# Kernel optimization log

Hardware: AMD Instinct MI355X
Metric: run time of the kernel (lower is better)

The kernel has to match this reference:

```python
import jax, jax.numpy as jnp
import numpy as np

D_MODEL = 768
NUM_HEADS = 12
HEAD_DIM = D_MODEL // NUM_HEADS
SEQ = 4096
BATCH = 1


def setup_inputs() -> dict:
    key = jax.random.key(0)
    ks = jax.random.split(key, 6)
    scale = 1.0 / np.sqrt(D_MODEL)
    x = jax.random.normal(ks[0], (BATCH, SEQ, D_MODEL), dtype=jnp.float32)
    mask = jnp.tril(jnp.ones((SEQ, SEQ), dtype=bool))[None, None]  # [1,1,S,S] causal
    Wq = jax.random.normal(ks[1], (D_MODEL, D_MODEL), dtype=jnp.float32) * scale
    Wk = jax.random.normal(ks[2], (D_MODEL, D_MODEL), dtype=jnp.float32) * scale
    Wv = jax.random.normal(ks[3], (D_MODEL, D_MODEL), dtype=jnp.float32) * scale
    Wo = jax.random.normal(ks[4], (D_MODEL, D_MODEL), dtype=jnp.float32) * scale
    bo = jax.random.normal(ks[5], (D_MODEL,), dtype=jnp.float32) * 0.01
    return {"x": x, "mask": mask, "Wq": Wq, "Wk": Wk, "Wv": Wv, "Wo": Wo, "bo": bo}


def _rope_tables(seq_len, head_dim, dtype):
    # inv_freq over even dims; emb = cat(freqs, freqs) but only the first half
    # participates in the well-defined rotation (x1/x2 have head_dim//2 channels)
    inv_freq = 1.0 / (10000.0 ** (jnp.arange(0, head_dim, 2, dtype=dtype) / head_dim))
    t = jnp.arange(seq_len, dtype=dtype)
    freqs = t[:, None] * inv_freq[None, :]  # [S, head_dim//2]
    return jnp.cos(freqs), jnp.sin(freqs)


def _apply_rotary(xh, cos, sin):
    # xh: [B,H,S,hd]; cos/sin: [S, hd//2]
    x1 = xh[..., ::2]
    x2 = xh[..., 1::2]
    # faithful to source: concatenated (not interleaved) rotated halves
    return jnp.concatenate([x1 * cos - x2 * sin, x1 * sin + x2 * cos], axis=-1)


def reference(x, mask, Wq, Wk, Wv, Wo, bo):
    B, S, D = x.shape
    H, hd = NUM_HEADS, HEAD_DIM
    def split_heads(y):
        return y.reshape(B, S, H, hd).transpose(0, 2, 1, 3)  # [B,H,S,hd]
    q = split_heads(x @ Wq.T)
    k = split_heads(x @ Wk.T)
    v = split_heads(x @ Wv.T)
    cos, sin = _rope_tables(S, hd, x.dtype)
    q = _apply_rotary(q, cos, sin)
    k = _apply_rotary(k, cos, sin)
    scores = jnp.einsum('bhqd,bhkd->bhqk', q, k) / jnp.sqrt(jnp.asarray(hd, x.dtype))
    scores = jnp.where(mask, scores, jnp.asarray(-1e9, x.dtype))
    attn = jax.nn.softmax(scores, axis=-1)  # dropout is identity in eval
    out = jnp.einsum('bhqk,bhkd->bhqd', attn, v)
    out = out.transpose(0, 2, 1, 3).reshape(B, S, D)
    return out @ Wo.T + bo
```

## Files before the change

### kernel.cpp

```cpp
#include <hip/hip_runtime.h>
#include <hip/hip_bf16.h>
#include <math.h>

#define SEQ 4096
#define DM  768
#define NH  12
#define HD  64
#define PER ((size_t)NH * SEQ * HD)
#define XN  ((size_t)SEQ * DM)
#define WN  ((size_t)DM * DM)

typedef __attribute__((ext_vector_type(8))) short bf16x8;
typedef __attribute__((ext_vector_type(4))) short s16x4;
typedef __attribute__((ext_vector_type(4))) float f32x4;

#define MFMA(a, b, c) __builtin_amdgcn_mfma_f32_16x16x32_bf16((a), (b), (c), 0, 0, 0)

#if __has_builtin(__builtin_amdgcn_exp2f)
#define EXP2(x) __builtin_amdgcn_exp2f(x)
#else
#define EXP2(x) exp2f(x)
#endif

#define SWZ(row, blk) (((row) << 6) + ((((blk) ^ ((row) & 7))) << 3))

__device__ __forceinline__ unsigned short f2b(float f) {
    unsigned int u = __float_as_uint(f);
    u += 0x7FFFu + ((u >> 16) & 1u);
    return (unsigned short)(u >> 16);
}

__global__ __launch_bounds__(256) void prep_kernel(
    const float* __restrict__ x,  const float* __restrict__ wq,
    const float* __restrict__ wk, const float* __restrict__ wv,
    const float* __restrict__ wo,
    unsigned short* __restrict__ dstbase, float2* __restrict__ rope)
{
    const float* srcs[5] = {x, wq, wk, wv, wo};
    const size_t n4s[5]  = {XN / 4, WN / 4, WN / 4, WN / 4, WN / 4};
    unsigned short* d = dstbase;
    for (int rg = 0; rg < 5; ++rg) {
        const float4* s4 = (const float4*)srcs[rg];
        s16x4* d4 = (s16x4*)d;
        for (size_t i = (size_t)blockIdx.x * 256 + threadIdx.x; i < n4s[rg];
             i += (size_t)gridDim.x * 256) {
            const float4 v = s4[i];
            s16x4 p;
            p.x = (short)f2b(v.x); p.y = (short)f2b(v.y);
            p.z = (short)f2b(v.z); p.w = (short)f2b(v.w);
            d4[i] = p;
        }
        d += n4s[rg] * 4;
    }
    for (int g = blockIdx.x * 256 + threadIdx.x; g < 131072; g += gridDim.x * 256) {
        const int row = g >> 5, fi = g & 31;
        const float invf = expf(-(float)fi * 0.28782313662425576f);
        float sn, cs;
        sincosf((float)row * invf, &sn, &cs);
        rope[row * 32 + fi] = make_float2(cs, sn);
    }
}

__global__ __launch_bounds__(256) void qkv128(
    const float* __restrict__ x,  const unsigned short* __restrict__ xb,
    const float* __restrict__ Wq, const float* __restrict__ Wk, const float* __restrict__ Wv,
    const unsigned short* __restrict__ Wqb, const unsigned short* __restrict__ Wkb,
    const unsigned short* __restrict__ Wvb,
    const float2* __restrict__ rope,
    unsigned short* __restrict__ Qo, unsigned short* __restrict__ Ko,
    unsigned short* __restrict__ Vo, int fast)
{
    __shared__ __align__(16) unsigned short SMEM[32768];
    unsigned short* At0 = SMEM;
    unsigned short* At1 = SMEM + 8192;
    unsigned short* Bt0 = SMEM + 16384;
    unsigned short* Bt1 = SMEM + 24576;

    const int t    = threadIdx.x;
    const int w    = t >> 6;
    const int lane = t & 63;
    const int quad = lane >> 4;
    const int l16  = lane & 15;
    const int region = blockIdx.y / 6;
    const int ntile  = blockIdx.y % 6;
    const int n0 = ntile * 128;
    const int s0 = blockIdx.x * 128;
    const int m0  = 64 * (w & 1);
    const int nn0 = 64 * (w >> 1);

    const unsigned short* Wb = (region == 0) ? Wqb : (region == 1) ? Wkb : Wvb;
    const float*          Wf = (region == 0) ? Wq  : (region == 1) ? Wk  : Wv;

    f32x4 acc[4][4];
    #pragma unroll
    for (int i = 0; i < 4; ++i)
        #pragma unroll
        for (int j = 0; j < 4; ++j) acc[i][j] = (f32x4){0, 0, 0, 0};

    bf16x8 areg[4], breg[4];
    if (fast) {
        #pragma unroll
        for (int i = 0; i < 4; ++i) {
            const int s = t + i * 256, row = s >> 3, bp = s & 7, blk = bp ^ (row & 7);
            areg[i] = *(const bf16x8*)&xb[(size_t)(s0 + row) * DM + blk * 8];
            breg[i] = *(const bf16x8*)&Wb[(size_t)(n0 + row) * DM + blk * 8];
        }
        #pragma unroll
        for (int i = 0; i < 4; ++i) {
            const int s = t + i * 256, row = s >> 3, bp = s & 7;
            *(bf16x8*)&At0[row * 64 + bp * 8] = areg[i];
            *(bf16x8*)&Bt0[row * 64 + bp * 8] = breg[i];
        }
    } else {
        for (int e = t; e < 2048; e += 256) {
            const int row = e >> 4, c4 = e & 15;
            const int off = (row << 6) + (((c4 >> 1) ^ (row & 7)) << 3) + (c4 & 1) * 4;
            const float4 xv = *(const float4*)&x[(size_t)(s0 + row) * DM + c4 * 4];
            s16x4 px; px.x = (short)f2b(xv.x); px.y = (short)f2b(xv.y);
            px.z = (short)f2b(xv.z); px.w = (short)f2b(xv.w);
            *(s16x4*)&At0[off] = px;
            const float4 wv = *(const float4*)&Wf[(size_t)(n0 + row) * DM + c4 * 4];
            s16x4 pw; pw.x = (short)f2b(wv.x); pw.y = (short)f2b(wv.y);
            pw.z = (short)f2b(wv.z); pw.w = (short)f2b(wv.w);
            *(s16x4*)&Bt0[off] = pw;
        }
    }
    __syncthreads();

    for (int kt = 0; kt < 12; ++kt) {
        if (fast && kt < 11) {
            const int k0n = (kt + 1) * 64;
            #pragma unroll
            for (int i = 0; i < 4; ++i) {
                const int s = t + i * 256, row = s >> 3, bp = s & 7, blk = bp ^ (row & 7);
                areg[i] = *(const bf16x8*)&xb[(size_t)(s0 + row) * DM + k0n + blk * 8];
                breg[i] = *(const bf16x8*)&Wb[(size_t)(n0 + row) * DM + k0n + blk * 8];
            }
        }
        const unsigned short* Ab = (kt & 1) ? At1 : At0;
        const unsigned short* Bb = (kt & 1) ? Bt1 : Bt0;

        bf16x8 aA[4][2], bB[4][2];
        #pragma unroll
        for (int i = 0; i < 4; ++i)
            #pragma unroll
            for (int hh = 0; hh < 2; ++hh) {
                aA[i][hh] = *(const bf16x8*)&Ab[SWZ(m0 + 16 * i + l16, 4 * hh + quad)];
                bB[i][hh] = *(const bf16x8*)&Bb[SWZ(nn0 + 16 * i + l16, 4 * hh + quad)];
            }
        #pragma unroll
        for (int hh = 0; hh < 2; ++hh)
            #pragma unroll
            for (int i = 0; i < 4; ++i)
                #pragma unroll
                for (int j = 0; j < 4; ++j)
                    acc[i][j] = MFMA(aA[i][hh], bB[j][hh], acc[i][j]);

        if (kt < 11) {
            unsigned short* An = ((kt + 1) & 1) ? At1 : At0;
            unsigned short* Bn = ((kt + 1) & 1) ? Bt1 : Bt0;
            if (fast) {
                #pragma unroll
                for (int i = 0; i < 4; ++i) {
                    const int s = t + i * 256, row = s >> 3, bp = s & 7;
                    *(bf16x8*)&An[row * 64 + bp * 8] = areg[i];
                    *(bf16x8*)&Bn[row * 64 + bp * 8] = breg[i];
                }
            } else {
                const int k0n = (kt + 1) * 64;
                for (int e = t; e < 2048; e += 256) {
                    const int row = e >> 4, c4 = e & 15;
                    const int off = (row << 6) + (((c4 >> 1) ^ (row & 7)) << 3) + (c4 & 1) * 4;
                    const float4 xv = *(const float4*)&x[(size_t)(s0 + row) * DM + k0n + c4 * 4];
                    s16x4 px; px.x = (short)f2b(xv.x); px.y = (short)f2b(xv.y);
                    px.z = (short)f2b(xv.z); px.w = (short)f2b(xv.w);
                    *(s16x4*)&An[off] = px;
                    const float4 wv = *(const float4*)&Wf[(size_t)(n0 + row) * DM + k0n + c4 * 4];
                    s16x4 pw; pw.x = (short)f2b(wv.x); pw.y = (short)f2b(wv.y);
                    pw.z = (short)f2b(wv.z); pw.w = (short)f2b(wv.w);
                    *(s16x4*)&Bn[off] = pw;
                }
            }
        }
        __syncthreads();
    }

    if (region <= 1) {
        unsigned short* dst = (region == 0) ? Qo : Ko;
        const float qsc = (region == 0) ? 0.18033688011112042f : 1.0f;
        #pragma unroll
        for (int i = 0; i < 4; ++i)
            #pragma unroll
            for (int j = 0; j < 4; ++j)
                #pragma unroll
                for (int r = 0; r < 4; ++r) {
                    const int srow = s0 + m0 + 16 * i + 4 * quad + r;
                    const int n = n0 + nn0 + 16 * j + l16;
                    const int h = n >> 6, d = n & 63, fi = d >> 1;
                    const float own = acc[i][j][r] * qsc;
                    const float oth = __shfl_xor(own, 1);
                    float cs, sn;
                    if (fast) {
                        const float2 t2 = rope[srow * 32 + fi];
                        cs = t2.x; sn = t2.y;
                    } else {
                        const float invf = expf(-(float)fi * 0.28782313662425576f);
                        sincosf((float)srow * invf, &sn, &cs);
                    }
                    const float val = (d & 1) ? (oth * sn + own * cs)
                                              : (own * cs - oth * sn);
                    dst[(size_t)h * SEQ * HD + (size_t)srow * HD +
                        ((d & 1) ? 32 : 0) + fi] = f2b(val);
                }
    } else {
        unsigned short* VL = SMEM;
        #pragma unroll
        for (int i = 0; i < 4; ++i)
            #pragma unroll
            for (int j = 0; j < 4; ++j)
                #pragma unroll
                for (int r = 0; r < 4; ++r)
                    VL[(nn0 + 16 * j + l16) * 130 + m0 + 16 * i + 4 * quad + r] =
                        f2b(acc[i][j][r]);
        __syncthreads();
        for (int e = t; e < 8192; e += 256) {
            const int dl = e >> 6, sp = e & 63;
            const unsigned int v = (unsigned int)VL[dl * 130 + 2 * sp] |
                                   ((unsigned int)VL[dl * 130 + 2 * sp + 1] << 16);
            const int n = n0 + dl, h = n >> 6, d = n & 63;
            *(unsigned int*)&Vo[(size_t)h * SEQ * HD + (size_t)d * SEQ + s0 + 2 * sp] = v;
        }
    }
}

__global__ __launch_bounds__(256, 2) void attn_mfma(
    const unsigned short* __restrict__ Q,
    const unsigned short* __restrict__ K,
    const unsigned short* __restrict__ V,
    unsigned short* __restrict__ O,
    float* __restrict__ Part)
{
    __shared__ __align__(16) unsigned char SM[53248];
    unsigned short* Kst = (unsigned short*)SM;
    unsigned short* Vt  = (unsigned short*)(SM + 16384);
    unsigned short* Ps  = (unsigned short*)(SM + 32768);
    float* ACC  = (float*)SM;
    float* ACC2 = (float*)(SM + 32768);
    float* Lx   = (float*)(SM + 51200);

    const int h  = blockIdx.y;
    const int xx = blockIdx.x;
    int i, kstart, nch, domask, partial, pslice;
    if (gridDim.x == 96) {
        if (xx < 64) {
            i = 63 - xx; kstart = 0;
            const int full = ((i * 64 + 63) >> 7) + 1;
            nch = full < 16 ? full : 16;
            domask  = (i <= 31);
            partial = (i >= 32); pslice = 0;
        } else {
            i = 127 - xx; kstart = 2048;
            nch = ((i * 64 + 63 - 2048) >> 7) + 1;
            domask = 1; partial = 1; pslice = 1;
        }
    } else {
        i = 63 - xx; kstart = 0;
        nch = ((i * 64 + 63) >> 7) + 1;
        domask = 1; partial = 0; pslice = 0;
    }
    const int q0 = i * 64;

    const int t    = threadIdx.x;
    const int w    = t >> 6;
    const int lane = t & 63;
    const int quad = lane >> 4;
    const int l16  = lane & 15;
    const size_t headoff = (size_t)h * SEQ * HD;

    for (int e = t; e < 512; e += 256) {
        const int row = e >> 3, bp = e & 7, blk = bp ^ (row & 7);
        *(bf16x8*)&Kst[row * 64 + bp * 8] =
            *(const bf16x8*)&Q[headoff + (size_t)(q0 + row) * HD + blk * 8];
    }
    __syncthreads();
    bf16x8 aQ[4][2];
    #pragma unroll
    for (int qt = 0; qt < 4; ++qt)
        #pragma unroll
        for (int hh = 0; hh < 2; ++hh)
            aQ[qt][hh] = *(const bf16x8*)&Kst[SWZ(16 * qt + l16, 4 * hh + quad)];
    __syncthreads();

    bf16x8 kreg[4], vreg[4];
    #pragma unroll
    for (int ii = 0; ii < 4; ++ii) {
        const int e = t + ii * 256, row = e >> 3, bp = e & 7, blk = bp ^ (row & 7);
        kreg[ii] = *(const bf16x8*)&K[headoff + (size_t)(kstart + row) * HD + blk * 8];
    }
    #pragma unroll
    for (int ii = 0; ii < 4; ++ii) {
        const int e = t + ii * 256, row = e >> 4, bp = e & 15, blk = bp ^ (row & 15);
        vreg[ii] = *(const bf16x8*)&V[headoff + (size_t)row * SEQ + kstart + blk * 8];
    }
    #pragma unroll
    for (int ii = 0; ii < 4; ++ii) {
        const int e = t + ii * 256, row = e >> 3, bp = e & 7;
        *(bf16x8*)&Kst[row * 64 + bp * 8] = kreg[ii];
    }
    #pragma unroll
    for (int ii = 0; ii < 4; ++ii) {
        const int e = t + ii * 256, row = e >> 4, bp = e & 15;
        *(bf16x8*)&Vt[row * 128 + bp * 8] = vreg[ii];
    }
    __syncthreads();

    bf16x8 ones;
    #pragma unroll
    for (int ii = 0; ii < 8; ++ii) ones[ii] = (short)0x3F80;

    f32x4 oT[4][4];
    #pragma unroll
    for (int dt = 0; dt < 4; ++dt)
        #pragma unroll
        for (int qt = 0; qt < 4; ++qt) oT[dt][qt] = (f32x4){0,0,0,0};
    f32x4 lT[4] = {{0,0,0,0},{0,0,0,0},{0,0,0,0},{0,0,0,0}};

    unsigned short* usp = Ps + w * 2560;

    for (int c = 0; c < nch; ++c) {
        const int k0 = kstart + c * 128;

        f32x4 sC[4][2];
        #pragma unroll
        for (int qt = 0; qt < 4; ++qt)
            #pragma unroll
            for (int kt = 0; kt < 2; ++kt) sC[qt][kt] = (f32x4){0,0,0,0};
        #pragma unroll
        for (int kt = 0; kt < 2; ++kt) {
            const int krow = 32 * w + 16 * kt + l16;
            #pragma unroll
            for (int hh = 0; hh < 2; ++hh) {
                const bf16x8 bK = *(const bf16x8*)&Kst[SWZ(krow, 4 * hh + quad)];
                #pragma unroll
                for (int qt = 0; qt < 4; ++qt)
                    sC[qt][kt] = MFMA(aQ[qt][hh], bK, sC[qt][kt]);
            }
        }

        if (c < nch - 1) {
            const int kn = k0 + 128;
            #pragma unroll
            for (int ii = 0; ii < 4; ++ii) {
                const int e = t + ii * 256, row = e >> 3, bp = e & 7, blk = bp ^ (row & 7);
                kreg[ii] = *(const bf16x8*)&K[headoff + (size_t)(kn + row) * HD + blk * 8];
            }
            #pragma unroll
            for (int ii = 0; ii < 4; ++ii) {
                const int e = t + ii * 256, row = e >> 4, bp = e & 15, blk = bp ^ (row & 15);
                vreg[ii] = *(const bf16x8*)&V[headoff + (size_t)row * SEQ + kn + blk * 8];
            }
        }

        if (domask && c == nch - 1) {
            #pragma unroll
            for (int kt = 0; kt < 2; ++kt) {
                const int key = k0 + 32 * w + 16 * kt + l16;
                #pragma unroll
                for (int qt = 0; qt < 4; ++qt)
                    #pragma unroll
                    for (int r = 0; r < 4; ++r)
                        if (key > q0 + 16 * qt + 4 * quad + r) sC[qt][kt][r] = -1e30f;
            }
        }

        #pragma unroll
        for (int qt = 0; qt < 4; ++qt)
            #pragma unroll
            for (int kt = 0; kt < 2; ++kt)
                #pragma unroll
                for (int r = 0; r < 4; ++r)
                    usp[(16 * qt + 4 * quad + r) * 40 + 16 * kt + l16] =
                        f2b(EXP2(sC[qt][kt][r]));
        asm volatile("s_waitcnt lgkmcnt(0)" ::: "memory");

        bf16x8 aV[4];
        #pragma unroll
        for (int dt = 0; dt < 4; ++dt) {
            const int row = 16 * dt + l16;
            aV[dt] = *(const bf16x8*)&Vt[row * 128 + (((4 * w + quad) ^ (row & 15)) << 3)];
        }
        #pragma unroll
        for (int qt = 0; qt < 4; ++qt) {
            const bf16x8 bP = *(const bf16x8*)&usp[(16 * qt + l16) * 40 + quad * 8];
            lT[qt] = MFMA(ones, bP, lT[qt]);
            #pragma unroll
            for (int dt = 0; dt < 4; ++dt)
                oT[dt][qt] = MFMA(aV[dt], bP, oT[dt][qt]);
        }

        __syncthreads();
        if (c < nch - 1) {
            #pragma unroll
            for (int ii = 0; ii < 4; ++ii) {
                const int e = t + ii * 256, row = e >> 3, bp = e & 7;
                *(bf16x8*)&Kst[row * 64 + bp * 8] = kreg[ii];
            }
            #pragma unroll
            for (int ii = 0; ii < 4; ++ii) {
                const int e = t + ii * 256, row = e >> 4, bp = e & 15;
                *(bf16x8*)&Vt[row * 128 + bp * 8] = vreg[ii];
            }
        }
        __syncthreads();
    }

    if (w != 0 && quad == 0) {
        #pragma unroll
        for (int qt = 0; qt < 4; ++qt)
            Lx[w * 64 + 16 * qt + l16] = lT[qt][0];
    }
    if (w == 1) {
        #pragma unroll
        for (int dt = 0; dt < 4; ++dt)
            #pragma unroll
            for (int qt = 0; qt < 4; ++qt)
                *(f32x4*)&ACC[(16 * qt + l16) * 72 + 16 * dt + 4 * quad] = oT[dt][qt];
    }
    __syncthreads();
    if (w == 0) {
        #pragma unroll
        for (int dt = 0; dt < 4; ++dt)
            #pragma unroll
            for (int qt = 0; qt < 4; ++qt)
                oT[dt][qt] += *(const f32x4*)&ACC[(16 * qt + l16) * 72 + 16 * dt + 4 * quad];
    }
    if (w == 2) {
        #pragma unroll
        for (int dt = 0; dt < 4; ++dt)
            #pragma unroll
            for (int qt = 0; qt < 4; ++qt)
                *(f32x4*)&ACC2[(16 * qt + l16) * 72 + 16 * dt + 4 * quad] = oT[dt][qt];
    }
    __syncthreads();
    if (w == 0) {
        #pragma unroll
        for (int dt = 0; dt < 4; ++dt)
            #pragma unroll
            for (int qt = 0; qt < 4; ++qt)
                oT[dt][qt] += *(const f32x4*)&ACC2[(16 * qt + l16) * 72 + 16 * dt + 4 * quad];
    }
    if (w == 3) {
        #pragma unroll
        for (int dt = 0; dt < 4; ++dt)
            #pragma unroll
            for (int qt = 0; qt < 4; ++qt)
                *(f32x4*)&ACC[(16 * qt + l16) * 72 + 16 * dt + 4 * quad] = oT[dt][qt];
    }
    __syncthreads();
    if (w == 0) {
        float ls[4];
        #pragma unroll
        for (int qt = 0; qt < 4; ++qt) {
            #pragma unroll
            for (int dt = 0; dt < 4; ++dt)
                oT[dt][qt] += *(const f32x4*)&ACC[(16 * qt + l16) * 72 + 16 * dt + 4 * quad];
            ls[qt] = lT[qt][0] + Lx[64 + 16 * qt + l16] +
                     Lx[128 + 16 * qt + l16] + Lx[192 + 16 * qt + l16];
        }
        if (!partial) {
            #pragma unroll
            for (int qt = 0; qt < 4; ++qt) {
                const float inv = 1.0f / ls[qt];
                const size_t rowoff = (size_t)(q0 + 16 * qt + l16) * DM + h * HD;
                #pragma unroll
                for (int dt = 0; dt < 4; ++dt) {
                    ushort4 u;
                    u.x = f2b(oT[dt][qt][0] * inv);
                    u.y = f2b(oT[dt][qt][1] * inv);
                    u.z = f2b(oT[dt][qt][2] * inv);
                    u.w = f2b(oT[dt][qt][3] * inv);
                    *(ushort4*)&O[rowoff + 16 * dt + 4 * quad] = u;
                }
            }
        } else {
            float* P = Part + (size_t)(((i - 32) * 12 + h) * 2 + pslice) * 4160;
            #pragma unroll
            for (int dt = 0; dt < 4; ++dt)
                #pragma unroll
                for (int qt = 0; qt < 4; ++qt)
                    *(f32x4*)&P[(16 * qt + l16) * 64 + 16 * dt + 4 * quad] = oT[dt][qt];
            if (quad == 0) {
                #pragma unroll
                for (int qt = 0; qt < 4; ++qt)
                    P[4096 + 16 * qt + l16] = ls[qt];
            }
        }
    }
}

__global__ __launch_bounds__(256) void reduce_attn(
    const float* __restrict__ Part, unsigned short* __restrict__ O)
{
    const int b  = blockIdx.x;
    const int i  = 32 + b / 12, h = b % 12;
    const int q0 = i * 64;
    const float* P0 = Part + (size_t)(b * 2 + 0) * 4160;
    const float* P1 = Part + (size_t)(b * 2 + 1) * 4160;
    __shared__ float linv[64];
    const int t = threadIdx.x;
    if (t < 64) linv[t] = 1.0f / (P0[4096 + t] + P1[4096 + t]);
    __syncthreads();
    for (int idx = t; idx < 4096; idx += 256) {
        const int q = idx >> 6, d = idx & 63;
        const float v = (P0[q * 64 + d] + P1[q * 64 + d]) * linv[q];
        O[(size_t)(q0 + q) * DM + h * HD + d] = f2b(v);
    }
}

__global__ __launch_bounds__(256) void proj128(
    const unsigned short* __restrict__ A,
    const float* __restrict__ Wo, const unsigned short* __restrict__ Wob,
    const float* __restrict__ bo,
    float* __restrict__ out, int fast)
{
    __shared__ __align__(16) unsigned short SMEM[32768];
    unsigned short* At0 = SMEM;
    unsigned short* At1 = SMEM + 8192;
    unsigned short* Bt0 = SMEM + 16384;
    unsigned short* Bt1 = SMEM + 24576;

    const int t    = threadIdx.x;
    const int w    = t >> 6;
    const int lane = t & 63;
    const int quad = lane >> 4;
    const int l16  = lane & 15;
    const int s0 = blockIdx.x * 128;
    const int n0 = blockIdx.y * 128;
    const int m0  = 64 * (w & 1);
    const int nn0 = 64 * (w >> 1);

    f32x4 acc[4][4];
    #pragma unroll
    for (int i = 0; i < 4; ++i)
        #pragma unroll
        for (int j = 0; j < 4; ++j) acc[i][j] = (f32x4){0, 0, 0, 0};

    bf16x8 areg[4], breg[4];
    #pragma unroll
    for (int i = 0; i < 4; ++i) {
        const int s = t + i * 256, row = s >> 3, bp = s & 7, blk = bp ^ (row & 7);
        areg[i] = *(const bf16x8*)&A[(size_t)(s0 + row) * DM + blk * 8];
        if (fast) breg[i] = *(const bf16x8*)&Wob[(size_t)(n0 + row) * DM + blk * 8];
    }
    #pragma unroll
    for (int i = 0; i < 4; ++i) {
        const int s = t + i * 256, row = s >> 3, bp = s & 7;
        *(bf16x8*)&At0[row * 64 + bp * 8] = areg[i];
        if (fast) *(bf16x8*)&Bt0[row * 64 + bp * 8] = breg[i];
    }
    if (!fast) {
        for (int e = t; e < 2048; e += 256) {
            const int row = e >> 4, c4 = e & 15;
            const int off = (row << 6) + (((c4 >> 1) ^ (row & 7)) << 3) + (c4 & 1) * 4;
            const float4 wv = *(const float4*)&Wo[(size_t)(n0 + row) * DM + c4 * 4];
            s16x4 pw; pw.x = (short)f2b(wv.x); pw.y = (short)f2b(wv.y);
            pw.z = (short)f2b(wv.z); pw.w = (short)f2b(wv.w);
            *(s16x4*)&Bt0[off] = pw;
        }
    }
    __syncthreads();

    for (int kt = 0; kt < 12; ++kt) {
        if (kt < 11) {
            const int k0n = (kt + 1) * 64;
            #pragma unroll
            for (int i = 0; i < 4; ++i) {
                const int s = t + i * 256, row = s >> 3, bp = s & 7, blk = bp ^ (row & 7);
                areg[i] = *(const bf16x8*)&A[(size_t)(s0 + row) * DM + k0n + blk * 8];
                if (fast) breg[i] = *(const bf16x8*)&Wob[(size_t)(n0 + row) * DM + k0n + blk * 8];
            }
        }
        const unsigned short* Ab = (kt & 1) ? At1 : At0;
        const unsigned short* Bb = (kt & 1) ? Bt1 : Bt0;

        bf16x8 aA[4][2], bB[4][2];
        #pragma unroll
        for (int i = 0; i < 4; ++i)
            #pragma unroll
            for (int hh = 0; hh < 2; ++hh) {
                aA[i][hh] = *(const bf16x8*)&Ab[SWZ(m0 + 16 * i + l16, 4 * hh + quad)];
                bB[i][hh] = *(const bf16x8*)&Bb[SWZ(nn0 + 16 * i + l16, 4 * hh + quad)];
            }
        #pragma unroll
        for (int hh = 0; hh < 2; ++hh)
            #pragma unroll
            for (int i = 0; i < 4; ++i)
                #pragma unroll
                for (int j = 0; j < 4; ++j)
                    acc[i][j] = MFMA(aA[i][hh], bB[j][hh], acc[i][j]);

        if (kt < 11) {
            unsigned short* An = ((kt + 1) & 1) ? At1 : At0;
            unsigned short* Bn = ((kt + 1) & 1) ? Bt1 : Bt0;
            #pragma unroll
            for (int i = 0; i < 4; ++i) {
                const int s = t + i * 256, row = s >> 3, bp = s & 7;
                *(bf16x8*)&An[row * 64 + bp * 8] = areg[i];
                if (fast) *(bf16x8*)&Bn[row * 64 + bp * 8] = breg[i];
            }
            if (!fast) {
                const int k0n = (kt + 1) * 64;
                for (int e = t; e < 2048; e += 256) {
                    const int row = e >> 4, c4 = e & 15;
                    const int off = (row << 6) + (((c4 >> 1) ^ (row & 7)) << 3) + (c4 & 1) * 4;
                    const float4 wv = *(const float4*)&Wo[(size_t)(n0 + row) * DM + k0n + c4 * 4];
                    s16x4 pw; pw.x = (short)f2b(wv.x); pw.y = (short)f2b(wv.y);
                    pw.z = (short)f2b(wv.z); pw.w = (short)f2b(wv.w);
                    *(s16x4*)&Bn[off] = pw;
                }
            }
        }
        __syncthreads();
    }

    #pragma unroll
    for (int i = 0; i < 4; ++i)
        #pragma unroll
        for (int j = 0; j < 4; ++j) {
            const int n = n0 + nn0 + 16 * j + l16;
            const float bv = bo[n];
            #pragma unroll
            for (int r = 0; r < 4; ++r) {
                const int srow = s0 + m0 + 16 * i + 4 * quad + r;
                out[(size_t)srow * DM + n] = acc[i][j][r] + bv;
            }
        }
}

extern "C" void kernel_launch(void* const* d_in, const int* in_sizes, int n_in,
                              void* d_out, int out_size, void* d_ws, size_t ws_size,
                              hipStream_t stream) {
    const float* x  = (const float*)d_in[0];
    const float* Wq = (const float*)d_in[2];
    const float* Wk = (const float*)d_in[3];
    const float* Wv = (const float*)d_in[4];
    const float* Wo = (const float*)d_in[5];
    const float* bo = (const float*)d_in[6];
    float* out = (float*)d_out;

    unsigned short* U  = (unsigned short*)d_ws;
    unsigned short* Qw = U;
    unsigned short* Kw = U + PER;
    unsigned short* Vw = U + 2 * PER;
    unsigned short* Ow = U + 3 * PER;
    unsigned short* xb  = U + 4 * PER;
    unsigned short* Wqb = xb + XN;
    unsigned short* Wkb = Wqb + WN;
    unsigned short* Wvb = Wkb + WN;
    unsigned short* Wob = Wvb + WN;
    float2* rope = (float2*)(Wob + WN);
    float*  part = (float*)(rope + 4096 * 32);
    const size_t need  = (char*)part - (char*)d_ws;
    const size_t need2 = need + (size_t)384 * 2 * 4160 * 4;
    const int fast  = (ws_size >= need)  ? 1 : 0;
    const int split = (ws_size >= need2) ? 1 : 0;

    if (fast)
        prep_kernel<<<1024, 256, 0, stream>>>(x, Wq, Wk, Wv, Wo, xb, rope);
    qkv128<<<dim3(SEQ / 128, 18), 256, 0, stream>>>(
        x, xb, Wq, Wk, Wv, Wqb, Wkb, Wvb, rope, Qw, Kw, Vw, fast);
    if (split) {
        attn_mfma<<<dim3(96, NH), 256, 0, stream>>>(Qw, Kw, Vw, Ow, part);
        reduce_attn<<<dim3(384), 256, 0, stream>>>(part, Ow);
    } else {
        attn_mfma<<<dim3(64, NH), 256, 0, stream>>>(Qw, Kw, Vw, Ow, part);
    }
    proj128<<<dim3(SEQ / 128, DM / 128), 256, 0, stream>>>(Ow, Wo, Wob, bo, out, fast);
}
```

Measured before the change: 246.5 us.

## Single-buffer QKV GEMM LDS, split V transpose, launch attention in head groups

The QKV GEMM kernel drops its double-buffered LDS tiles for a single 32 KB buffer, adding an extra barrier per k-step after fragments are read. The LDS footprint drops so more blocks can share a CU. The V-transpose epilogue is done in two 64-column passes so it fits the smaller buffer. The split attention launch is broken into three launches of four heads each through a new head-base argument, which changes scheduling and adds launch overhead.

```diff
diff --git a/kernel.cpp b/kernel.cpp
--- a/kernel.cpp
+++ b/kernel.cpp
@@ -70,11 +70,9 @@
     unsigned short* __restrict__ Qo, unsigned short* __restrict__ Ko,
     unsigned short* __restrict__ Vo, int fast)
 {
-    __shared__ __align__(16) unsigned short SMEM[32768];
-    unsigned short* At0 = SMEM;
-    unsigned short* At1 = SMEM + 8192;
-    unsigned short* Bt0 = SMEM + 16384;
-    unsigned short* Bt1 = SMEM + 24576;
+    __shared__ __align__(16) unsigned short SMEM[16384];
+    unsigned short* At = SMEM;
+    unsigned short* Bt = SMEM + 8192;
 
     const int t    = threadIdx.x;
     const int w    = t >> 6;
@@ -108,8 +106,8 @@
         #pragma unroll
         for (int i = 0; i < 4; ++i) {
             const int s = t + i * 256, row = s >> 3, bp = s & 7;
-            *(bf16x8*)&At0[row * 64 + bp * 8] = areg[i];
-            *(bf16x8*)&Bt0[row * 64 + bp * 8] = breg[i];
+            *(bf16x8*)&At[row * 64 + bp * 8] = areg[i];
+            *(bf16x8*)&Bt[row * 64 + bp * 8] = breg[i];
         }
     } else {
         for (int e = t; e < 2048; e += 256) {
@@ -118,11 +116,11 @@
             const float4 xv = *(const float4*)&x[(size_t)(s0 + row) * DM + c4 * 4];
             s16x4 px; px.x = (short)f2b(xv.x); px.y = (short)f2b(xv.y);
             px.z = (short)f2b(xv.z); px.w = (short)f2b(xv.w);
-            *(s16x4*)&At0[off] = px;
+            *(s16x4*)&At[off] = px;
             const float4 wv = *(const float4*)&Wf[(size_t)(n0 + row) * DM + c4 * 4];
             s16x4 pw; pw.x = (short)f2b(wv.x); pw.y = (short)f2b(wv.y);
             pw.z = (short)f2b(wv.z); pw.w = (short)f2b(wv.w);
-            *(s16x4*)&Bt0[off] = pw;
+            *(s16x4*)&Bt[off] = pw;
         }
     }
     __syncthreads();
@@ -137,17 +135,16 @@
                 breg[i] = *(const bf16x8*)&Wb[(size_t)(n0 + row) * DM + k0n + blk * 8];
             }
         }
-        const unsigned short* Ab = (kt & 1) ? At1 : At0;
-        const unsigned short* Bb = (kt & 1) ? Bt1 : Bt0;
-
         bf16x8 aA[4][2], bB[4][2];
         #pragma unroll
         for (int i = 0; i < 4; ++i)
             #pragma unroll
             for (int hh = 0; hh < 2; ++hh) {
-                aA[i][hh] = *(const bf16x8*)&Ab[SWZ(m0 + 16 * i + l16, 4 * hh + quad)];
-                bB[i][hh] = *(const bf16x8*)&Bb[SWZ(nn0 + 16 * i + l16, 4 * hh + quad)];
-            }
+                aA[i][hh] = *(const bf16x8*)&At[SWZ(m0 + 16 * i + l16, 4 * hh + quad)];
+                bB[i][hh] = *(const bf16x8*)&Bt[SWZ(nn0 + 16 * i + l16, 4 * hh + quad)];
+            }
+        __syncthreads();
+
         #pragma unroll
         for (int hh = 0; hh < 2; ++hh)
             #pragma unroll
@@ -157,14 +154,12 @@
                     acc[i][j] = MFMA(aA[i][hh], bB[j][hh], acc[i][j]);
 
         if (kt < 11) {
-            unsigned short* An = ((kt + 1) & 1) ? At1 : At0;
-            unsigned short* Bn = ((kt + 1) & 1) ? Bt1 : Bt0;
             if (fast) {
                 #pragma unroll
                 for (int i = 0; i < 4; ++i) {
                     const int s = t + i * 256, row = s >> 3, bp = s & 7;
-                    *(bf16x8*)&An[row * 64 + bp * 8] = areg[i];
-                    *(bf16x8*)&Bn[row * 64 + bp * 8] = breg[i];
+                    *(bf16x8*)&At[row * 64 + bp * 8] = areg[i];
+                    *(bf16x8*)&Bt[row * 64 + bp * 8] = breg[i];
                 }
             } else {
                 const int k0n = (kt + 1) * 64;
@@ -174,11 +169,11 @@
                     const float4 xv = *(const float4*)&x[(size_t)(s0 + row) * DM + k0n + c4 * 4];
                     s16x4 px; px.x = (short)f2b(xv.x); px.y = (short)f2b(xv.y);
                     px.z = (short)f2b(xv.z); px.w = (short)f2b(xv.w);
-                    *(s16x4*)&An[off] = px;
+                    *(s16x4*)&At[off] = px;
                     const float4 wv = *(const float4*)&Wf[(size_t)(n0 + row) * DM + k0n + c4 * 4];
                     s16x4 pw; pw.x = (short)f2b(wv.x); pw.y = (short)f2b(wv.y);
                     pw.z = (short)f2b(wv.z); pw.w = (short)f2b(wv.w);
-                    *(s16x4*)&Bn[off] = pw;
+                    *(s16x4*)&Bt[off] = pw;
                 }
             }
         }
@@ -215,20 +210,26 @@
     } else {
         unsigned short* VL = SMEM;
         #pragma unroll
-        for (int i = 0; i < 4; ++i)
-            #pragma unroll
-            for (int j = 0; j < 4; ++j)
-                #pragma unroll
-                for (int r = 0; r < 4; ++r)
-                    VL[(nn0 + 16 * j + l16) * 130 + m0 + 16 * i + 4 * quad + r] =
-                        f2b(acc[i][j][r]);
-        __syncthreads();
-        for (int e = t; e < 8192; e += 256) {
-            const int dl = e >> 6, sp = e & 63;
-            const unsigned int v = (unsigned int)VL[dl * 130 + 2 * sp] |
-                                   ((unsigned int)VL[dl * 130 + 2 * sp + 1] << 16);
-            const int n = n0 + dl, h = n >> 6, d = n & 63;
-            *(unsigned int*)&Vo[(size_t)h * SEQ * HD + (size_t)d * SEQ + s0 + 2 * sp] = v;
+        for (int p = 0; p < 2; ++p) {
+            if ((w >> 1) == p) {
+                #pragma unroll
+                for (int i = 0; i < 4; ++i)
+                    #pragma unroll
+                    for (int j = 0; j < 4; ++j)
+                        #pragma unroll
+                        for (int r = 0; r < 4; ++r)
+                            VL[(16 * j + l16) * 130 + m0 + 16 * i + 4 * quad + r] =
+                                f2b(acc[i][j][r]);
+            }
+            __syncthreads();
+            for (int e = t; e < 4096; e += 256) {
+                const int dl = e >> 6, sp = e & 63;
+                const unsigned int v = (unsigned int)VL[dl * 130 + 2 * sp] |
+                                       ((unsigned int)VL[dl * 130 + 2 * sp + 1] << 16);
+                const int n = n0 + 64 * p + dl, h = n >> 6, d = n & 63;
+                *(unsigned int*)&Vo[(size_t)h * SEQ * HD + (size_t)d * SEQ + s0 + 2 * sp] = v;
+            }
+            __syncthreads();
         }
     }
 }
@@ -238,7 +239,8 @@
     const unsigned short* __restrict__ K,
     const unsigned short* __restrict__ V,
     unsigned short* __restrict__ O,
-    float* __restrict__ Part)
+    float* __restrict__ Part,
+    int hbase)
 {
     __shared__ __align__(16) unsigned char SM[53248];
     unsigned short* Kst = (unsigned short*)SM;
@@ -248,7 +250,7 @@
     float* ACC2 = (float*)(SM + 32768);
     float* Lx   = (float*)(SM + 51200);
 
-    const int h  = blockIdx.y;
+    const int h  = hbase + blockIdx.y;
     const int xx = blockIdx.x;
     int i, kstart, nch, domask, partial, pslice;
     if (gridDim.x == 96) {
@@ -670,10 +672,12 @@
     qkv128<<<dim3(SEQ / 128, 18), 256, 0, stream>>>(
         x, xb, Wq, Wk, Wv, Wqb, Wkb, Wvb, rope, Qw, Kw, Vw, fast);
     if (split) {
-        attn_mfma<<<dim3(96, NH), 256, 0, stream>>>(Qw, Kw, Vw, Ow, part);
+        attn_mfma<<<dim3(96, 4), 256, 0, stream>>>(Qw, Kw, Vw, Ow, part, 0);
+        attn_mfma<<<dim3(96, 4), 256, 0, stream>>>(Qw, Kw, Vw, Ow, part, 4);
+        attn_mfma<<<dim3(96, 4), 256, 0, stream>>>(Qw, Kw, Vw, Ow, part, 8);
         reduce_attn<<<dim3(384), 256, 0, stream>>>(part, Ow);
     } else {
-        attn_mfma<<<dim3(64, NH), 256, 0, stream>>>(Qw, Kw, Vw, Ow, part);
+        attn_mfma<<<dim3(64, NH), 256, 0, stream>>>(Qw, Kw, Vw, Ow, part, 0);
     }
     proj128<<<dim3(SEQ / 128, DM / 128), 256, 0, stream>>>(Ow, Wo, Wob, bo, out, fast);
 }
```

Measured after the change: 264.0 us. 1.07x slower.
